# Optimization experiments

Hardware: AMD Instinct MI355X
Metric: run time of the kernel (lower is better)

Reference implementation:

```python
import jax, jax.numpy as jnp
import numpy as np

N, E, D, B, C = 50000, 800000, 128, 20000, 40
EPS_BN = 1e-3    # keras BatchNormalization default epsilon
EPS_NRM = 1e-12  # keras ops.nn.normalize epsilon
FFN_DIMS = {"pre": (D, D), "c1p": (D, D), "c1u": (2 * D, D), "c2p": (D, D), "c2u": (2 * D, D), "post": (D, D)}


def setup_inputs() -> dict:
    key = jax.random.key(0)
    ks = jax.random.split(key, 8)
    inp = {
        "node_features": jax.random.normal(ks[0], (N, D), jnp.float32),
        "edges": jax.random.randint(ks[1], (2, E), 0, N, dtype=jnp.int32),
        "edge_w": jax.random.uniform(ks[2], (E,), jnp.float32),
        "input_node_idx": jax.random.randint(ks[3], (B,), 0, N, dtype=jnp.int32),
    }
    for i, (name, (din, dout)) in enumerate(FFN_DIMS.items()):
        kw = jax.random.fold_in(key, 100 + i)
        inp[name + "_g"] = jnp.ones((din,), jnp.float32)
        inp[name + "_be"] = jnp.zeros((din,), jnp.float32)
        inp[name + "_mu"] = jnp.zeros((din,), jnp.float32)
        inp[name + "_var"] = jnp.ones((din,), jnp.float32)
        inp[name + "_w"] = jax.random.normal(kw, (din, dout), jnp.float32) * (1.0 / float(np.sqrt(din)))
        inp[name + "_bi"] = jnp.zeros((dout,), jnp.float32)
    inp["logits_w"] = jax.random.normal(ks[4], (D, C), jnp.float32) * (1.0 / float(np.sqrt(D)))
    inp["logits_b"] = jnp.zeros((C,), jnp.float32)
    return inp


def ffn(x, g, be, mu, var, w, bi):
    # BatchNorm (inference running stats) -> Dropout (identity) -> Dense + exact gelu
    xn = (x - mu) * jax.lax.rsqrt(var + EPS_BN) * g + be
    return jax.nn.gelu(xn @ w + bi, approximate=False)


def l2norm(x):
    n = jnp.sqrt(jnp.sum(x * x, axis=-1, keepdims=True))
    return x / jnp.maximum(n, EPS_NRM)


def graph_conv(x, node_idx, nbr_idx, ew, prep, upd):
    # gather neighbours -> prepare FFN -> edge-weighted -> segment_sum (reduce='sum')
    msgs = ffn(x[nbr_idx], *prep) * ew[:, None]                         # [E, D]
    red = jax.ops.segment_sum(msgs, node_idx, num_segments=x.shape[0])  # [N, D]
    h = jnp.concatenate([x, red], axis=1)                               # [N, 2D] (combination='concat')
    return l2norm(ffn(h, *upd))                                         # normalize=True


def reference(node_features, edges, edge_w, input_node_idx,
              pre_g, pre_be, pre_mu, pre_var, pre_w, pre_bi,
              c1p_g, c1p_be, c1p_mu, c1p_var, c1p_w, c1p_bi,
              c1u_g, c1u_be, c1u_mu, c1u_var, c1u_w, c1u_bi,
              c2p_g, c2p_be, c2p_mu, c2p_var, c2p_w, c2p_bi,
              c2u_g, c2u_be, c2u_mu, c2u_var, c2u_w, c2u_bi,
              post_g, post_be, post_mu, post_var, post_w, post_bi,
              logits_w, logits_b):
    ew = edge_w / jnp.sum(edge_w)                       # edge_W normalized at init
    node_idx, nbr_idx = edges[0], edges[1]
    x = ffn(node_features, pre_g, pre_be, pre_mu, pre_var, pre_w, pre_bi)
    x = graph_conv(x, node_idx, nbr_idx, ew,
                   (c1p_g, c1p_be, c1p_mu, c1p_var, c1p_w, c1p_bi),
                   (c1u_g, c1u_be, c1u_mu, c1u_var, c1u_w, c1u_bi)) + x
    x = graph_conv(x, node_idx, nbr_idx, ew,
                   (c2p_g, c2p_be, c2p_mu, c2p_var, c2p_w, c2p_bi),
                   (c2u_g, c2u_be, c2u_mu, c2u_var, c2u_w, c2u_bi)) + x
    x = ffn(x, post_g, post_be, post_mu, post_var, post_w, post_bi)
    return x[input_node_idx] @ logits_w + logits_b      # [B, C]
```

## Files before the change

### kernel.cpp

```cpp
#include <hip/hip_runtime.h>
#include <hip/hip_fp16.h>
#include <math.h>

static constexpr int D = 128;
static constexpr int CAP = 64;
static constexpr int ST = 40;
static constexpr float EPS_BN = 1e-3f;

typedef short short8 __attribute__((ext_vector_type(8)));
typedef short short4v __attribute__((ext_vector_type(4)));
typedef float float4v __attribute__((ext_vector_type(4)));

__device__ __forceinline__ float gelu_exact(float x) {
    return 0.5f * x * (1.0f + erff(x * 0.70710678118654752f));
}

__device__ __forceinline__ void f32_to_hilo(float f, short& h, short& l) {
    unsigned u = __float_as_uint(f);
    h = (short)(u >> 16);
    float hf = __uint_as_float(u & 0xFFFF0000u);
    unsigned lu = __float_as_uint(f - hf);
    l = (short)(lu >> 16);
}

__device__ __forceinline__ short f32_to_bf16_rne(float f) {
    unsigned u = __float_as_uint(f);
    u += 0x7FFFu + ((u >> 16) & 1u);
    return (short)(u >> 16);
}

struct FoldArgs {
    const float* g[6]; const float* be[6]; const float* mu[6];
    const float* var[6]; const float* w[6]; const float* bi[6];
    short* wh[6]; short* wl[6]; float* bp[6]; int K[6];
};

__global__ void k_build(const int* __restrict__ edges, const float* __restrict__ ew,
                        int* __restrict__ cnt, float* __restrict__ sums,
                        unsigned* __restrict__ cw, FoldArgs fa, int E, int N, int fillBlocks) {
    __shared__ float sm[4];
    const int tid = threadIdx.x;
    const int lane = tid & 63, wvi = tid >> 6;

    if ((int)blockIdx.x < fillBlocks) {
        const int g = blockIdx.x & 7;
        const int bid = blockIdx.x >> 3;
        const int gstride = (fillBlocks >> 3) * 256;
        const int N8 = (N + 7) >> 3;
        const int lo = g * N8;
        const int hi = min(lo + N8, N);
        float s = 0.f;
        for (int e = bid * 256 + tid; e < E; e += gstride) {
            int dst = edges[e];
            if (dst >= lo && dst < hi) {
                int src = edges[E + e];
                float w = ew[e];
                s += w;
                unsigned short wb = __half_as_ushort(__float2half(w));
                int idx = atomicAdd(&cnt[dst], 1);
                if (idx < CAP)
                    cw[(size_t)dst * CAP + idx] = ((unsigned)src << 16) | (unsigned)wb;
            }
        }
        for (int off = 32; off > 0; off >>= 1) s += __shfl_down(s, off, 64);
        if (lane == 0) sm[wvi] = s;
        __syncthreads();
        if (tid == 0) {
            float t = sm[0] + sm[1] + sm[2] + sm[3];
            if (t != 0.f) atomicAdd(sums, t);
        }
    } else {
        const int idx = blockIdx.x - fillBlocks;
        const int f = idx >> 7;
        const int c = idx & 127;
        const int K = fa.K[f];
        const float* g = fa.g[f]; const float* be = fa.be[f];
        const float* mu = fa.mu[f]; const float* var = fa.var[f];
        const float* w = fa.w[f]; const float* bi = fa.bi[f];
        short* wh = fa.wh[f]; short* wl = fa.wl[f]; float* bp = fa.bp[f];
        float part = 0.f;
        for (int k = tid; k < K; k += blockDim.x) {
            float a = g[k] / sqrtf(var[k] + EPS_BN);
            float wv = w[k * D + c];
            float prod = a * wv;
            short hh, ll;
            f32_to_hilo(prod, hh, ll);
            wh[c * K + k] = hh;
            wl[c * K + k] = ll;
            part += (be[k] - mu[k] * a) * wv;
        }
        for (int off = 32; off > 0; off >>= 1) part += __shfl_down(part, off, 64);
        if (lane == 0) sm[wvi] = part;
        __syncthreads();
        if (tid == 0) bp[c] = bi[c] + sm[0] + sm[1] + sm[2] + sm[3];
    }
}

__global__ void k_reduce(const int* __restrict__ cnt, const unsigned* __restrict__ cw,
                         const __half* __restrict__ y, __half* __restrict__ red, int N) {
    int n = blockIdx.x * (blockDim.x >> 6) + (threadIdx.x >> 6);
    if (n >= N) return;
    int lane = threadIdx.x & 63;
    int sub = lane >> 4;
    int q = lane & 15;
    int count = min(cnt[n], CAP);
    int start = n * CAP;
    int end = start + count;
    float acc[8] = {0.f, 0.f, 0.f, 0.f, 0.f, 0.f, 0.f, 0.f};
    int i = start + sub;
    if (i < end) {
        unsigned c = cw[i];
        for (;;) {
            int ni = i + 4;
            unsigned nc = 0;
            if (ni < end) nc = cw[ni];
            int src = (int)(c >> 16);
            float w = __half2float(__ushort_as_half((unsigned short)(c & 0xFFFFu)));
            float4 raw = *((const float4*)(y + (size_t)src * D) + q);
            const __half2* hp = (const __half2*)&raw;
            #pragma unroll
            for (int t = 0; t < 4; t++) {
                float2 f = __half22float2(hp[t]);
                acc[t * 2]     += w * f.x;
                acc[t * 2 + 1] += w * f.y;
            }
            if (ni >= end) break;
            i = ni; c = nc;
        }
    }
    #pragma unroll
    for (int t = 0; t < 8; t++) {
        acc[t] += __shfl_xor(acc[t], 16, 64);
        acc[t] += __shfl_xor(acc[t], 32, 64);
    }
    if (sub == 0) {
        float4 ov;
        __half2* op = (__half2*)&ov;
        #pragma unroll
        for (int t = 0; t < 4; t++)
            op[t] = __floats2half2_rn(acc[t * 2], acc[t * 2 + 1]);
        *((float4*)(red + (size_t)n * D + q * 8)) = ov;
    }
}

template<int K, bool L2RES, bool OUT16, bool SPLIT3>
__device__ __forceinline__ void ffn_body(
    short (*__restrict__ Abuf)[128][ST], short (*__restrict__ Wbuf)[128][ST],
    float (*__restrict__ rs)[2], int rowBlock,
    const float* __restrict__ A0, const __half* __restrict__ A1,
    const float* __restrict__ sums,
    const short* __restrict__ Wh, const short* __restrict__ Wl,
    const float* __restrict__ bp, const float* __restrict__ resid,
    float* __restrict__ outf, __half* __restrict__ outh, int nrows)
{
    const int tid = threadIdx.x;
    const int lane = tid & 63;
    const int wv = tid >> 6;
    const int wr = wv >> 1;
    const int wc = wv & 1;
    const int m = lane & 15;
    const int quad = lane >> 4;

    float inv = 1.0f;
    if (K == 256) inv = 1.0f / sums[0];

    float4v acc[4][4];
    #pragma unroll
    for (int ti = 0; ti < 4; ti++)
        #pragma unroll
        for (int tj = 0; tj < 4; tj++)
            acc[ti][tj] = (float4v){0.f, 0.f, 0.f, 0.f};

    for (int cc = 0; cc < K / 32; cc++) {
        const int kw = cc * 32;
        const bool useA1 = (K == 256 && cc >= 4);
        const int kb = (K == 256) ? ((cc & 3) * 32) : kw;

        if (!useA1) {
            #pragma unroll
            for (int t = 0; t < 4; t++) {
                int i = tid + t * 256;
                int r = i >> 3, k4 = i & 7;
                int grow = rowBlock + r; if (grow >= nrows) grow = nrows - 1;
                float4 f = *((const float4*)(A0 + (size_t)grow * D + kb) + k4);
                if (SPLIT3) {
                    short h0, l0, h1, l1, h2, l2, h3, l3;
                    f32_to_hilo(f.x, h0, l0);
                    f32_to_hilo(f.y, h1, l1);
                    f32_to_hilo(f.z, h2, l2);
                    f32_to_hilo(f.w, h3, l3);
                    short4v hh = {h0, h1, h2, h3};
                    short4v ll = {l0, l1, l2, l3};
                    *(short4v*)&Abuf[0][r][k4 * 4] = hh;
                    *(short4v*)&Abuf[1][r][k4 * 4] = ll;
                } else {
                    short4v hh = {f32_to_bf16_rne(f.x), f32_to_bf16_rne(f.y),
                                  f32_to_bf16_rne(f.z), f32_to_bf16_rne(f.w)};
                    *(short4v*)&Abuf[0][r][k4 * 4] = hh;
                }
            }
        } else {
            #pragma unroll
            for (int t = 0; t < 2; t++) {
                int i = tid + t * 256;
                int r = i >> 2, g8 = i & 3;
                int grow = rowBlock + r; if (grow >= nrows) grow = nrows - 1;
                float4 raw = *((const float4*)(A1 + (size_t)grow * D + kb) + g8);
                const __half2* hp = (const __half2*)&raw;
                short hs[8], ls[8];
                #pragma unroll
                for (int j = 0; j < 4; j++) {
                    float2 fv = __half22float2(hp[j]);
                    f32_to_hilo(fv.x * inv, hs[2 * j], ls[2 * j]);
                    f32_to_hilo(fv.y * inv, hs[2 * j + 1], ls[2 * j + 1]);
                }
                short8 hv = {hs[0], hs[1], hs[2], hs[3], hs[4], hs[5], hs[6], hs[7]};
                short8 lv = {ls[0], ls[1], ls[2], ls[3], ls[4], ls[5], ls[6], ls[7]};
                *(short8*)&Abuf[0][r][g8 * 8] = hv;
                *(short8*)&Abuf[1][r][g8 * 8] = lv;
            }
        }
        #pragma unroll
        for (int t = 0; t < 2; t++) {
            int i = tid + t * 256;
            int c = i >> 2, g = i & 3;
            *(short8*)&Wbuf[0][c][g * 8] = *(const short8*)(Wh + (size_t)c * K + kw + g * 8);
            if (SPLIT3)
                *(short8*)&Wbuf[1][c][g * 8] = *(const short8*)(Wl + (size_t)c * K + kw + g * 8);
        }
        __syncthreads();

        short8 ah[4], bh[4];
        #pragma unroll
        for (int ti = 0; ti < 4; ti++)
            ah[ti] = *(const short8*)&Abuf[0][wr * 64 + ti * 16 + m][quad * 8];
        #pragma unroll
        for (int tj = 0; tj < 4; tj++)
            bh[tj] = *(const short8*)&Wbuf[0][wc * 64 + tj * 16 + m][quad * 8];
        if (SPLIT3) {
            short8 al[4], bl[4];
            #pragma unroll
            for (int ti = 0; ti < 4; ti++)
                al[ti] = *(const short8*)&Abuf[1][wr * 64 + ti * 16 + m][quad * 8];
            #pragma unroll
            for (int tj = 0; tj < 4; tj++)
                bl[tj] = *(const short8*)&Wbuf[1][wc * 64 + tj * 16 + m][quad * 8];
            #pragma unroll
            for (int ti = 0; ti < 4; ti++)
                #pragma unroll
                for (int tj = 0; tj < 4; tj++) {
                    acc[ti][tj] = __builtin_amdgcn_mfma_f32_16x16x32_bf16(al[ti], bh[tj], acc[ti][tj], 0, 0, 0);
                    acc[ti][tj] = __builtin_amdgcn_mfma_f32_16x16x32_bf16(ah[ti], bl[tj], acc[ti][tj], 0, 0, 0);
                    acc[ti][tj] = __builtin_amdgcn_mfma_f32_16x16x32_bf16(ah[ti], bh[tj], acc[ti][tj], 0, 0, 0);
                }
        } else {
            #pragma unroll
            for (int ti = 0; ti < 4; ti++)
                #pragma unroll
                for (int tj = 0; tj < 4; tj++)
                    acc[ti][tj] = __builtin_amdgcn_mfma_f32_16x16x32_bf16(ah[ti], bh[tj], acc[ti][tj], 0, 0, 0);
        }
        __syncthreads();
    }

    float bvv[4];
    #pragma unroll
    for (int tj = 0; tj < 4; tj++) bvv[tj] = bp[wc * 64 + tj * 16 + m];

    float g[4][4][4];
    #pragma unroll
    for (int ti = 0; ti < 4; ti++)
        #pragma unroll
        for (int tj = 0; tj < 4; tj++)
            #pragma unroll
            for (int r4 = 0; r4 < 4; r4++)
                g[ti][tj][r4] = gelu_exact(acc[ti][tj][r4] + bvv[tj]);

    if (L2RES) {
        #pragma unroll
        for (int ti = 0; ti < 4; ti++)
            #pragma unroll
            for (int r4 = 0; r4 < 4; r4++) {
                float ss = 0.f;
                #pragma unroll
                for (int tj = 0; tj < 4; tj++) ss += g[ti][tj][r4] * g[ti][tj][r4];
                ss += __shfl_xor(ss, 1, 64);
                ss += __shfl_xor(ss, 2, 64);
                ss += __shfl_xor(ss, 4, 64);
                ss += __shfl_xor(ss, 8, 64);
                if (m == 0) rs[wr * 64 + ti * 16 + quad * 4 + r4][wc] = ss;
            }
        __syncthreads();
        #pragma unroll
        for (int ti = 0; ti < 4; ti++)
            #pragma unroll
            for (int r4 = 0; r4 < 4; r4++) {
                int rib = wr * 64 + ti * 16 + quad * 4 + r4;
                float tot = rs[rib][0] + rs[rib][1];
                float invn = 1.0f / fmaxf(sqrtf(tot), 1e-12f);
                int row = rowBlock + rib;
                if (row < nrows) {
                    #pragma unroll
                    for (int tj = 0; tj < 4; tj++) {
                        int c = wc * 64 + tj * 16 + m;
                        outf[(size_t)row * D + c] = g[ti][tj][r4] * invn + resid[(size_t)row * D + c];
                    }
                }
            }
    } else {
        #pragma unroll
        for (int ti = 0; ti < 4; ti++)
            #pragma unroll
            for (int r4 = 0; r4 < 4; r4++) {
                int row = rowBlock + wr * 64 + ti * 16 + quad * 4 + r4;
                if (row < nrows) {
                    #pragma unroll
                    for (int tj = 0; tj < 4; tj++) {
                        int c = wc * 64 + tj * 16 + m;
                        if (OUT16) outh[(size_t)row * D + c] = __float2half(g[ti][tj][r4]);
                        else       outf[(size_t)row * D + c] = g[ti][tj][r4];
                    }
                }
            }
    }
}

__global__ __launch_bounds__(256, 3) void k_pair1(
    const float* __restrict__ nf,
    const short* __restrict__ Wh0, const short* __restrict__ Wl0, const float* __restrict__ Bp0,
    float* __restrict__ xA,
    const short* __restrict__ Wh1, const float* __restrict__ Bp1,
    __half* __restrict__ yh, int N)
{
    __shared__ short Abuf[2][128][ST];
    __shared__ short Wbuf[2][128][ST];
    __shared__ float rs[128][2];
    int rowBlock = blockIdx.x * 128;
    ffn_body<128, false, false, true>(Abuf, Wbuf, rs, rowBlock, nf, nullptr, nullptr, Wh0, Wl0, Bp0, nullptr, xA, nullptr, N);
    __syncthreads();
    ffn_body<128, false, true, false>(Abuf, Wbuf, rs, rowBlock, xA, nullptr, nullptr, Wh1, nullptr, Bp1, nullptr, nullptr, yh, N);
}

__global__ __launch_bounds__(256, 3) void k_pair2(
    const float* __restrict__ xA, const __half* __restrict__ red, const float* __restrict__ sums,
    const short* __restrict__ Wh2, const short* __restrict__ Wl2, const float* __restrict__ Bp2,
    float* __restrict__ y,
    const short* __restrict__ Wh3, const float* __restrict__ Bp3,
    __half* __restrict__ yh, int N)
{
    __shared__ short Abuf[2][128][ST];
    __shared__ short Wbuf[2][128][ST];
    __shared__ float rs[128][2];
    int rowBlock = blockIdx.x * 128;
    ffn_body<256, true, false, true>(Abuf, Wbuf, rs, rowBlock, xA, red, sums, Wh2, Wl2, Bp2, xA, y, nullptr, N);
    __syncthreads();
    ffn_body<128, false, true, false>(Abuf, Wbuf, rs, rowBlock, y, nullptr, nullptr, Wh3, nullptr, Bp3, nullptr, nullptr, yh, N);
}

__global__ __launch_bounds__(256, 3) void k_pair3(
    const float* __restrict__ y, const __half* __restrict__ red, const float* __restrict__ sums,
    const short* __restrict__ Wh4, const short* __restrict__ Wl4, const float* __restrict__ Bp4,
    float* __restrict__ xA,
    const short* __restrict__ Wh5, const short* __restrict__ Wl5, const float* __restrict__ Bp5,
    __half* __restrict__ yh, int N)
{
    __shared__ short Abuf[2][128][ST];
    __shared__ short Wbuf[2][128][ST];
    __shared__ float rs[128][2];
    int rowBlock = blockIdx.x * 128;
    ffn_body<256, true, false, true>(Abuf, Wbuf, rs, rowBlock, y, red, sums, Wh4, Wl4, Bp4, y, xA, nullptr, N);
    __syncthreads();
    ffn_body<128, false, true, true>(Abuf, Wbuf, rs, rowBlock, xA, nullptr, nullptr, Wh5, Wl5, Bp5, nullptr, nullptr, yh, N);
}

__global__ void k_logits(const __half* __restrict__ x, const int* __restrict__ idx,
                         const float* __restrict__ LW, const float* __restrict__ lb,
                         float* __restrict__ out, int B) {
    int wid = blockIdx.x * 4 + (threadIdx.x >> 6);
    int lane = threadIdx.x & 63;
    if (wid >= B) return;
    int row = __builtin_amdgcn_readfirstlane(idx[wid]);
    if (lane >= 40) return;
    float acc = lb[lane];
    const float4* xr = (const float4*)(x + (size_t)row * D);
    #pragma unroll 4
    for (int k8 = 0; k8 < 16; k8++) {
        float4 raw = xr[k8];
        const __half2* hp = (const __half2*)&raw;
        #pragma unroll
        for (int j = 0; j < 4; j++) {
            float2 f = __half22float2(hp[j]);
            acc += f.x * LW[(k8 * 8 + 2 * j) * 40 + lane];
            acc += f.y * LW[(k8 * 8 + 2 * j + 1) * 40 + lane];
        }
    }
    out[(size_t)wid * 40 + lane] = acc;
}

extern "C" void kernel_launch(void* const* d_in, const int* in_sizes, int n_in,
                              void* d_out, int out_size, void* d_ws, size_t ws_size,
                              hipStream_t stream) {
    const float* node_features = (const float*)d_in[0];
    const int*   edges         = (const int*)d_in[1];
    const float* edge_w        = (const float*)d_in[2];
    const int*   input_idx     = (const int*)d_in[3];
    const int N = in_sizes[0] / D;
    const int E = in_sizes[2];
    const int B = in_sizes[3];

    const float* P[6][6];
    for (int f = 0; f < 6; f++)
        for (int q = 0; q < 6; q++)
            P[f][q] = (const float*)d_in[4 + f * 6 + q];
    const float* logits_w = (const float*)d_in[40];
    const float* logits_b = (const float*)d_in[41];

    float* ws = (float*)d_ws;
    size_t nd = (size_t)N * D;
    float* xA  = ws;
    float* y   = ws + nd;
    float* p   = ws + 2 * nd;
    __half* redh = (__half*)p; p += nd / 2;
    __half* yh   = (__half*)p; p += nd / 2;
    const int Ks[6] = {128, 128, 256, 128, 256, 128};
    short* Wh[6]; short* Wl[6]; float* Bp[6];
    {
        short* sp = (short*)p;
        for (int f = 0; f < 6; f++) {
            Wh[f] = sp; sp += (size_t)Ks[f] * D;
            Wl[f] = sp; sp += (size_t)Ks[f] * D;
        }
        p = (float*)sp;
    }
    for (int f = 0; f < 6; f++) { Bp[f] = p; p += D; }
    int* cnt    = (int*)p; p += N;
    float* sums = p; p += 2;
    unsigned* cw = (unsigned*)p; p += (size_t)N * CAP;

    FoldArgs fa;
    for (int f = 0; f < 6; f++) {
        fa.g[f] = P[f][0]; fa.be[f] = P[f][1]; fa.mu[f] = P[f][2];
        fa.var[f] = P[f][3]; fa.w[f] = P[f][4]; fa.bi[f] = P[f][5];
        fa.wh[f] = Wh[f]; fa.wl[f] = Wl[f]; fa.bp[f] = Bp[f]; fa.K[f] = Ks[f];
    }

    const int gb = (N + 127) / 128;
    const int rb = (N + 3) / 4;
    const int FB = 1024;

    hipMemsetAsync(cnt, 0, ((size_t)N + 2) * sizeof(int), stream);
    k_build<<<FB + 768, 256, 0, stream>>>(edges, edge_w, cnt, sums, cw, fa, E, N, FB);

    k_pair1<<<gb, 256, 0, stream>>>(node_features, Wh[0], Wl[0], Bp[0], xA, Wh[1], Bp[1], yh, N);
    k_reduce<<<rb, 256, 0, stream>>>(cnt, cw, yh, redh, N);
    k_pair2<<<gb, 256, 0, stream>>>(xA, redh, sums, Wh[2], Wl[2], Bp[2], y, Wh[3], Bp[3], yh, N);
    k_reduce<<<rb, 256, 0, stream>>>(cnt, cw, yh, redh, N);
    k_pair3<<<gb, 256, 0, stream>>>(y, redh, sums, Wh[4], Wl[4], Bp[4], xA, Wh[5], Wl[5], Bp[5], yh, N);
    k_logits<<<(B + 3) / 4, 256, 0, stream>>>(yh, input_idx, logits_w, logits_b, (float*)d_out, B);
}
```

Measured before the change: 476.9 us.

## Drop split-bf16 GEMMs for plain bf16, store activations in bf16, widen K tile

Removes the hi/lo bf16 split (three MFMAs per tile) in all FFN GEMMs and uses single bf16 weights and activations. Intermediate node activations xA/y are stored as bf16 instead of fp32, halving their traffic. The K chunk is widened from 32 to 64 with single LDS buffers and occupancy raised to 4 blocks per SM. Logits weights are staged in shared memory. This trades accuracy (bf16 rounding of residual stream and weights) for fewer MFMAs and less memory traffic, which may exceed tolerance.

```diff
diff --git a/kernel.cpp b/kernel.cpp
--- a/kernel.cpp
+++ b/kernel.cpp
@@ -4,7 +4,7 @@
 
 static constexpr int D = 128;
 static constexpr int CAP = 64;
-static constexpr int ST = 40;
+static constexpr int ST = 72;
 static constexpr float EPS_BN = 1e-3f;
 
 typedef short short8 __attribute__((ext_vector_type(8)));
@@ -13,14 +13,6 @@
 
 __device__ __forceinline__ float gelu_exact(float x) {
     return 0.5f * x * (1.0f + erff(x * 0.70710678118654752f));
-}
-
-__device__ __forceinline__ void f32_to_hilo(float f, short& h, short& l) {
-    unsigned u = __float_as_uint(f);
-    h = (short)(u >> 16);
-    float hf = __uint_as_float(u & 0xFFFF0000u);
-    unsigned lu = __float_as_uint(f - hf);
-    l = (short)(lu >> 16);
 }
 
 __device__ __forceinline__ short f32_to_bf16_rne(float f) {
@@ -29,10 +21,14 @@
     return (short)(u >> 16);
 }
 
+__device__ __forceinline__ float bf16_to_f32(short s) {
+    return __uint_as_float(((unsigned)(unsigned short)s) << 16);
+}
+
 struct FoldArgs {
     const float* g[6]; const float* be[6]; const float* mu[6];
     const float* var[6]; const float* w[6]; const float* bi[6];
-    short* wh[6]; short* wl[6]; float* bp[6]; int K[6];
+    short* wh[6]; float* bp[6]; int K[6];
 };
 
 __global__ void k_build(const int* __restrict__ edges, const float* __restrict__ ew,
@@ -77,16 +73,12 @@
         const float* g = fa.g[f]; const float* be = fa.be[f];
         const float* mu = fa.mu[f]; const float* var = fa.var[f];
         const float* w = fa.w[f]; const float* bi = fa.bi[f];
-        short* wh = fa.wh[f]; short* wl = fa.wl[f]; float* bp = fa.bp[f];
+        short* wh = fa.wh[f]; float* bp = fa.bp[f];
         float part = 0.f;
         for (int k = tid; k < K; k += blockDim.x) {
             float a = g[k] / sqrtf(var[k] + EPS_BN);
             float wv = w[k * D + c];
-            float prod = a * wv;
-            short hh, ll;
-            f32_to_hilo(prod, hh, ll);
-            wh[c * K + k] = hh;
-            wl[c * K + k] = ll;
+            wh[c * K + k] = f32_to_bf16_rne(a * wv);
             part += (be[k] - mu[k] * a) * wv;
         }
         for (int off = 32; off > 0; off >>= 1) part += __shfl_down(part, off, 64);
@@ -143,15 +135,15 @@
     }
 }
 
-template<int K, bool L2RES, bool OUT16, bool SPLIT3>
+template<int K, bool L2RES, bool OUT16, bool FP32A>
 __device__ __forceinline__ void ffn_body(
-    short (*__restrict__ Abuf)[128][ST], short (*__restrict__ Wbuf)[128][ST],
+    short (*__restrict__ Abuf)[ST], short (*__restrict__ Wbuf)[ST],
     float (*__restrict__ rs)[2], int rowBlock,
-    const float* __restrict__ A0, const __half* __restrict__ A1,
-    const float* __restrict__ sums,
-    const short* __restrict__ Wh, const short* __restrict__ Wl,
-    const float* __restrict__ bp, const float* __restrict__ resid,
-    float* __restrict__ outf, __half* __restrict__ outh, int nrows)
+    const float* __restrict__ A0f, const short* __restrict__ A0b,
+    const __half* __restrict__ A1, const float* __restrict__ sums,
+    const short* __restrict__ Wh, const float* __restrict__ bp,
+    const short* __restrict__ residb,
+    short* __restrict__ outb, __half* __restrict__ outh, int nrows)
 {
     const int tid = threadIdx.x;
     const int lane = tid & 63;
@@ -171,89 +163,66 @@
         for (int tj = 0; tj < 4; tj++)
             acc[ti][tj] = (float4v){0.f, 0.f, 0.f, 0.f};
 
-    for (int cc = 0; cc < K / 32; cc++) {
-        const int kw = cc * 32;
-        const bool useA1 = (K == 256 && cc >= 4);
-        const int kb = (K == 256) ? ((cc & 3) * 32) : kw;
-
-        if (!useA1) {
+    for (int cc = 0; cc < K / 64; cc++) {
+        const int kw = cc * 64;
+        const bool useA1 = (K == 256 && cc >= 2);
+        const int kb = (K == 256) ? ((cc & 1) * 64) : kw;
+
+        if (FP32A && !useA1) {
+            #pragma unroll
+            for (int t = 0; t < 8; t++) {
+                int i = tid + t * 256;
+                int r = i >> 4, k4 = i & 15;
+                int grow = rowBlock + r; if (grow >= nrows) grow = nrows - 1;
+                float4 f = *((const float4*)(A0f + (size_t)grow * D + kb) + k4);
+                short4v hh = {f32_to_bf16_rne(f.x), f32_to_bf16_rne(f.y),
+                              f32_to_bf16_rne(f.z), f32_to_bf16_rne(f.w)};
+                *(short4v*)&Abuf[r][k4 * 4] = hh;
+            }
+        } else if (!useA1) {
             #pragma unroll
             for (int t = 0; t < 4; t++) {
                 int i = tid + t * 256;
-                int r = i >> 3, k4 = i & 7;
+                int r = i >> 3, g8 = i & 7;
                 int grow = rowBlock + r; if (grow >= nrows) grow = nrows - 1;
-                float4 f = *((const float4*)(A0 + (size_t)grow * D + kb) + k4);
-                if (SPLIT3) {
-                    short h0, l0, h1, l1, h2, l2, h3, l3;
-                    f32_to_hilo(f.x, h0, l0);
-                    f32_to_hilo(f.y, h1, l1);
-                    f32_to_hilo(f.z, h2, l2);
-                    f32_to_hilo(f.w, h3, l3);
-                    short4v hh = {h0, h1, h2, h3};
-                    short4v ll = {l0, l1, l2, l3};
-                    *(short4v*)&Abuf[0][r][k4 * 4] = hh;
-                    *(short4v*)&Abuf[1][r][k4 * 4] = ll;
-                } else {
-                    short4v hh = {f32_to_bf16_rne(f.x), f32_to_bf16_rne(f.y),
-                                  f32_to_bf16_rne(f.z), f32_to_bf16_rne(f.w)};
-                    *(short4v*)&Abuf[0][r][k4 * 4] = hh;
-                }
+                *(short8*)&Abuf[r][g8 * 8] = *(const short8*)(A0b + (size_t)grow * D + kb + g8 * 8);
             }
         } else {
             #pragma unroll
-            for (int t = 0; t < 2; t++) {
+            for (int t = 0; t < 4; t++) {
                 int i = tid + t * 256;
-                int r = i >> 2, g8 = i & 3;
+                int r = i >> 3, g8 = i & 7;
                 int grow = rowBlock + r; if (grow >= nrows) grow = nrows - 1;
                 float4 raw = *((const float4*)(A1 + (size_t)grow * D + kb) + g8);
                 const __half2* hp = (const __half2*)&raw;
-                short hs[8], ls[8];
+                short hs[8];
                 #pragma unroll
                 for (int j = 0; j < 4; j++) {
                     float2 fv = __half22float2(hp[j]);
-                    f32_to_hilo(fv.x * inv, hs[2 * j], ls[2 * j]);
-                    f32_to_hilo(fv.y * inv, hs[2 * j + 1], ls[2 * j + 1]);
+                    hs[2 * j]     = f32_to_bf16_rne(fv.x * inv);
+                    hs[2 * j + 1] = f32_to_bf16_rne(fv.y * inv);
                 }
                 short8 hv = {hs[0], hs[1], hs[2], hs[3], hs[4], hs[5], hs[6], hs[7]};
-                short8 lv = {ls[0], ls[1], ls[2], ls[3], ls[4], ls[5], ls[6], ls[7]};
-                *(short8*)&Abuf[0][r][g8 * 8] = hv;
-                *(short8*)&Abuf[1][r][g8 * 8] = lv;
-            }
-        }
-        #pragma unroll
-        for (int t = 0; t < 2; t++) {
+                *(short8*)&Abuf[r][g8 * 8] = hv;
+            }
+        }
+        #pragma unroll
+        for (int t = 0; t < 4; t++) {
             int i = tid + t * 256;
-            int c = i >> 2, g = i & 3;
-            *(short8*)&Wbuf[0][c][g * 8] = *(const short8*)(Wh + (size_t)c * K + kw + g * 8);
-            if (SPLIT3)
-                *(short8*)&Wbuf[1][c][g * 8] = *(const short8*)(Wl + (size_t)c * K + kw + g * 8);
+            int c = i >> 3, g8 = i & 7;
+            *(short8*)&Wbuf[c][g8 * 8] = *(const short8*)(Wh + (size_t)c * K + kw + g8 * 8);
         }
         __syncthreads();
 
-        short8 ah[4], bh[4];
-        #pragma unroll
-        for (int ti = 0; ti < 4; ti++)
-            ah[ti] = *(const short8*)&Abuf[0][wr * 64 + ti * 16 + m][quad * 8];
-        #pragma unroll
-        for (int tj = 0; tj < 4; tj++)
-            bh[tj] = *(const short8*)&Wbuf[0][wc * 64 + tj * 16 + m][quad * 8];
-        if (SPLIT3) {
-            short8 al[4], bl[4];
+        #pragma unroll
+        for (int ks = 0; ks < 2; ks++) {
+            short8 ah[4], bh[4];
             #pragma unroll
             for (int ti = 0; ti < 4; ti++)
-                al[ti] = *(const short8*)&Abuf[1][wr * 64 + ti * 16 + m][quad * 8];
+                ah[ti] = *(const short8*)&Abuf[wr * 64 + ti * 16 + m][ks * 32 + quad * 8];
             #pragma unroll
             for (int tj = 0; tj < 4; tj++)
-                bl[tj] = *(const short8*)&Wbuf[1][wc * 64 + tj * 16 + m][quad * 8];
-            #pragma unroll
-            for (int ti = 0; ti < 4; ti++)
-                #pragma unroll
-                for (int tj = 0; tj < 4; tj++) {
-                    acc[ti][tj] = __builtin_amdgcn_mfma_f32_16x16x32_bf16(al[ti], bh[tj], acc[ti][tj], 0, 0, 0);
-                    acc[ti][tj] = __builtin_amdgcn_mfma_f32_16x16x32_bf16(ah[ti], bl[tj], acc[ti][tj], 0, 0, 0);
-                    acc[ti][tj] = __builtin_amdgcn_mfma_f32_16x16x32_bf16(ah[ti], bh[tj], acc[ti][tj], 0, 0, 0);
-                }
-        } else {
+                bh[tj] = *(const short8*)&Wbuf[wc * 64 + tj * 16 + m][ks * 32 + quad * 8];
             #pragma unroll
             for (int ti = 0; ti < 4; ti++)
                 #pragma unroll
@@ -303,7 +272,8 @@
                     #pragma unroll
                     for (int tj = 0; tj < 4; tj++) {
                         int c = wc * 64 + tj * 16 + m;
-                        outf[(size_t)row * D + c] = g[ti][tj][r4] * invn + resid[(size_t)row * D + c];
+                        float v = g[ti][tj][r4] * invn + bf16_to_f32(residb[(size_t)row * D + c]);
+                        outb[(size_t)row * D + c] = f32_to_bf16_rne(v);
                     }
                 }
             }
@@ -318,64 +288,67 @@
                     for (int tj = 0; tj < 4; tj++) {
                         int c = wc * 64 + tj * 16 + m;
                         if (OUT16) outh[(size_t)row * D + c] = __float2half(g[ti][tj][r4]);
-                        else       outf[(size_t)row * D + c] = g[ti][tj][r4];
+                        else       outb[(size_t)row * D + c] = f32_to_bf16_rne(g[ti][tj][r4]);
                     }
                 }
             }
     }
 }
 
-__global__ __launch_bounds__(256, 3) void k_pair1(
+__global__ __launch_bounds__(256, 4) void k_pair1(
     const float* __restrict__ nf,
-    const short* __restrict__ Wh0, const short* __restrict__ Wl0, const float* __restrict__ Bp0,
-    float* __restrict__ xA,
+    const short* __restrict__ Wh0, const float* __restrict__ Bp0,
+    short* __restrict__ xA,
     const short* __restrict__ Wh1, const float* __restrict__ Bp1,
     __half* __restrict__ yh, int N)
 {
-    __shared__ short Abuf[2][128][ST];
-    __shared__ short Wbuf[2][128][ST];
+    __shared__ short Abuf[128][ST];
+    __shared__ short Wbuf[128][ST];
     __shared__ float rs[128][2];
     int rowBlock = blockIdx.x * 128;
-    ffn_body<128, false, false, true>(Abuf, Wbuf, rs, rowBlock, nf, nullptr, nullptr, Wh0, Wl0, Bp0, nullptr, xA, nullptr, N);
+    ffn_body<128, false, false, true>(Abuf, Wbuf, rs, rowBlock, nf, nullptr, nullptr, nullptr, Wh0, Bp0, nullptr, xA, nullptr, N);
     __syncthreads();
-    ffn_body<128, false, true, false>(Abuf, Wbuf, rs, rowBlock, xA, nullptr, nullptr, Wh1, nullptr, Bp1, nullptr, nullptr, yh, N);
-}
-
-__global__ __launch_bounds__(256, 3) void k_pair2(
-    const float* __restrict__ xA, const __half* __restrict__ red, const float* __restrict__ sums,
-    const short* __restrict__ Wh2, const short* __restrict__ Wl2, const float* __restrict__ Bp2,
-    float* __restrict__ y,
+    ffn_body<128, false, true, false>(Abuf, Wbuf, rs, rowBlock, nullptr, xA, nullptr, nullptr, Wh1, Bp1, nullptr, nullptr, yh, N);
+}
+
+__global__ __launch_bounds__(256, 4) void k_pair2(
+    const short* __restrict__ xA, const __half* __restrict__ red, const float* __restrict__ sums,
+    const short* __restrict__ Wh2, const float* __restrict__ Bp2,
+    short* __restrict__ y,
     const short* __restrict__ Wh3, const float* __restrict__ Bp3,
     __half* __restrict__ yh, int N)
 {
-    __shared__ short Abuf[2][128][ST];
-    __shared__ short Wbuf[2][128][ST];
+    __shared__ short Abuf[128][ST];
+    __shared__ short Wbuf[128][ST];
     __shared__ float rs[128][2];
     int rowBlock = blockIdx.x * 128;
-    ffn_body<256, true, false, true>(Abuf, Wbuf, rs, rowBlock, xA, red, sums, Wh2, Wl2, Bp2, xA, y, nullptr, N);
+    ffn_body<256, true, false, false>(Abuf, Wbuf, rs, rowBlock, nullptr, xA, red, sums, Wh2, Bp2, xA, y, nullptr, N);
     __syncthreads();
-    ffn_body<128, false, true, false>(Abuf, Wbuf, rs, rowBlock, y, nullptr, nullptr, Wh3, nullptr, Bp3, nullptr, nullptr, yh, N);
-}
-
-__global__ __launch_bounds__(256, 3) void k_pair3(
-    const float* __restrict__ y, const __half* __restrict__ red, const float* __restrict__ sums,
-    const short* __restrict__ Wh4, const short* __restrict__ Wl4, const float* __restrict__ Bp4,
-    float* __restrict__ xA,
-    const short* __restrict__ Wh5, const short* __restrict__ Wl5, const float* __restrict__ Bp5,
+    ffn_body<128, false, true, false>(Abuf, Wbuf, rs, rowBlock, nullptr, y, nullptr, nullptr, Wh3, Bp3, nullptr, nullptr, yh, N);
+}
+
+__global__ __launch_bounds__(256, 4) void k_pair3(
+    const short* __restrict__ y, const __half* __restrict__ red, const float* __restrict__ sums,
+    const short* __restrict__ Wh4, const float* __restrict__ Bp4,
+    short* __restrict__ xA,
+    const short* __restrict__ Wh5, const float* __restrict__ Bp5,
     __half* __restrict__ yh, int N)
 {
-    __shared__ short Abuf[2][128][ST];
-    __shared__ short Wbuf[2][128][ST];
+    __shared__ short Abuf[128][ST];
+    __shared__ short Wbuf[128][ST];
     __shared__ float rs[128][2];
     int rowBlock = blockIdx.x * 128;
-    ffn_body<256, true, false, true>(Abuf, Wbuf, rs, rowBlock, y, red, sums, Wh4, Wl4, Bp4, y, xA, nullptr, N);
+    ffn_body<256, true, false, false>(Abuf, Wbuf, rs, rowBlock, nullptr, y, red, sums, Wh4, Bp4, y, xA, nullptr, N);
     __syncthreads();
-    ffn_body<128, false, true, true>(Abuf, Wbuf, rs, rowBlock, xA, nullptr, nullptr, Wh5, Wl5, Bp5, nullptr, nullptr, yh, N);
+    ffn_body<128, false, true, false>(Abuf, Wbuf, rs, rowBlock, nullptr, xA, nullptr, nullptr, Wh5, Bp5, nullptr, nullptr, yh, N);
 }
 
 __global__ void k_logits(const __half* __restrict__ x, const int* __restrict__ idx,
                          const float* __restrict__ LW, const float* __restrict__ lb,
                          float* __restrict__ out, int B) {
+    __shared__ float LWs[128 * 40];
+    for (int i = threadIdx.x; i < 128 * 40; i += 256) LWs[i] = LW[i];
+    __syncthreads();
     int wid = blockIdx.x * 4 + (threadIdx.x >> 6);
     int lane = threadIdx.x & 63;
     if (wid >= B) return;
@@ -390,8 +363,8 @@
         #pragma unroll
         for (int j = 0; j < 4; j++) {
             float2 f = __half22float2(hp[j]);
-            acc += f.x * LW[(k8 * 8 + 2 * j) * 40 + lane];
-            acc += f.y * LW[(k8 * 8 + 2 * j + 1) * 40 + lane];
+            acc += f.x * LWs[(k8 * 8 + 2 * j) * 40 + lane];
+            acc += f.y * LWs[(k8 * 8 + 2 * j + 1) * 40 + lane];
         }
     }
     out[(size_t)wid * 40 + lane] = acc;
@@ -415,33 +388,26 @@
     const float* logits_w = (const float*)d_in[40];
     const float* logits_b = (const float*)d_in[41];
 
-    float* ws = (float*)d_ws;
     size_t nd = (size_t)N * D;
-    float* xA  = ws;
-    float* y   = ws + nd;
-    float* p   = ws + 2 * nd;
-    __half* redh = (__half*)p; p += nd / 2;
-    __half* yh   = (__half*)p; p += nd / 2;
+    char* base = (char*)d_ws;
+    short* xA = (short*)base;            base += nd * sizeof(short);
+    short* y  = (short*)base;            base += nd * sizeof(short);
+    __half* redh = (__half*)base;        base += nd * sizeof(__half);
+    __half* yh   = (__half*)base;        base += nd * sizeof(__half);
     const int Ks[6] = {128, 128, 256, 128, 256, 128};
-    short* Wh[6]; short* Wl[6]; float* Bp[6];
-    {
-        short* sp = (short*)p;
-        for (int f = 0; f < 6; f++) {
-            Wh[f] = sp; sp += (size_t)Ks[f] * D;
-            Wl[f] = sp; sp += (size_t)Ks[f] * D;
-        }
-        p = (float*)sp;
-    }
-    for (int f = 0; f < 6; f++) { Bp[f] = p; p += D; }
-    int* cnt    = (int*)p; p += N;
-    float* sums = p; p += 2;
-    unsigned* cw = (unsigned*)p; p += (size_t)N * CAP;
+    short* Wh[6];
+    for (int f = 0; f < 6; f++) { Wh[f] = (short*)base; base += (size_t)Ks[f] * D * sizeof(short); }
+    float* Bp[6];
+    for (int f = 0; f < 6; f++) { Bp[f] = (float*)base; base += D * sizeof(float); }
+    int* cnt = (int*)base;               base += (size_t)N * sizeof(int);
+    float* sums = (float*)base;          base += 2 * sizeof(float);
+    unsigned* cw = (unsigned*)base;      base += (size_t)N * CAP * sizeof(unsigned);
 
     FoldArgs fa;
     for (int f = 0; f < 6; f++) {
         fa.g[f] = P[f][0]; fa.be[f] = P[f][1]; fa.mu[f] = P[f][2];
         fa.var[f] = P[f][3]; fa.w[f] = P[f][4]; fa.bi[f] = P[f][5];
-        fa.wh[f] = Wh[f]; fa.wl[f] = Wl[f]; fa.bp[f] = Bp[f]; fa.K[f] = Ks[f];
+        fa.wh[f] = Wh[f]; fa.bp[f] = Bp[f]; fa.K[f] = Ks[f];
     }
 
     const int gb = (N + 127) / 128;
@@ -451,10 +417,10 @@
     hipMemsetAsync(cnt, 0, ((size_t)N + 2) * sizeof(int), stream);
     k_build<<<FB + 768, 256, 0, stream>>>(edges, edge_w, cnt, sums, cw, fa, E, N, FB);
 
-    k_pair1<<<gb, 256, 0, stream>>>(node_features, Wh[0], Wl[0], Bp[0], xA, Wh[1], Bp[1], yh, N);
+    k_pair1<<<gb, 256, 0, stream>>>(node_features, Wh[0], Bp[0], xA, Wh[1], Bp[1], yh, N);
     k_reduce<<<rb, 256, 0, stream>>>(cnt, cw, yh, redh, N);
-    k_pair2<<<gb, 256, 0, stream>>>(xA, redh, sums, Wh[2], Wl[2], Bp[2], y, Wh[3], Bp[3], yh, N);
+    k_pair2<<<gb, 256, 0, stream>>>(xA, redh, sums, Wh[2], Bp[2], y, Wh[3], Bp[3], yh, N);
     k_reduce<<<rb, 256, 0, stream>>>(cnt, cw, yh, redh, N);
-    k_pair3<<<gb, 256, 0, stream>>>(y, redh, sums, Wh[4], Wl[4], Bp[4], xA, Wh[5], Wl[5], Bp[5], yh, N);
+    k_pair3<<<gb, 256, 0, stream>>>(y, redh, sums, Wh[4], Bp[4], xA, Wh[5], Bp[5], yh, N);
     k_logits<<<(B + 3) / 4, 256, 0, stream>>>(yh, input_idx, logits_w, logits_b, (float*)d_out, B);
 }
```

After: 523.5 us. 9.8% more time.
